# Kernel optimization log

Hardware: AMD Instinct MI355X
Metric: run time of the kernel (lower is better)

The kernel has to match this reference:

```python
import jax, jax.numpy as jnp
import numpy as np

N, E, D = 50000, 800000, 128
NODE_IN, EDGE_IN, STEPS = 19, 4, 5
EPS = 1e-5

def leaky(x):
    return jnp.where(x > 0, x, 0.05 * x)

def mlp3(x, W1, b1, W2, b2, W3, b3):
    x = leaky(x @ W1 + b1)
    x = leaky(x @ W2 + b2)
    return x @ W3 + b3

def layer_norm(x, g, b):
    m = jnp.mean(x, axis=-1, keepdims=True)
    v = jnp.var(x, axis=-1, keepdims=True)
    return (x - m) * jax.lax.rsqrt(v + EPS) * g + b

def batch_norm(x, g, b):
    # training-mode BatchNorm1d: biased batch stats over node dim
    m = jnp.mean(x, axis=0)
    v = jnp.var(x, axis=0)
    return (x - m) * jax.lax.rsqrt(v + EPS) * g + b

def gcn_conv(x, src, dst, W, b):
    # PyG GCNConv: add self loops, sym-normalize by deg^{-1/2}, aggregate at dst
    h = x @ W  # [N, D]
    deg = jax.ops.segment_sum(jnp.ones(E, x.dtype), dst, num_segments=N) + 1.0
    dis = jax.lax.rsqrt(deg)
    msg = h[src] * (dis[src] * dis[dst])[:, None]  # [E, D]
    agg = jax.ops.segment_sum(msg, dst, num_segments=N) + h * (dis * dis)[:, None]
    return agg + b


def setup_inputs() -> dict:
    key = jax.random.key(0)
    ks = iter(jax.random.split(key, 64))
    w = lambda shape: jax.random.normal(next(ks), shape, jnp.float32) * 0.05
    z = lambda: jnp.zeros((D,), jnp.float32)
    o = lambda: jnp.ones((D,), jnp.float32)
    inp = {
        'node_feat': jax.random.normal(next(ks), (N, NODE_IN), jnp.float32),
        'edge_feat': jax.random.normal(next(ks), (E, EDGE_IN), jnp.float32),
        'edge_index': jax.random.randint(next(ks), (2, E), 0, N, jnp.int32),
        'enc_node_W1': w((NODE_IN, D)), 'enc_node_b1': z(),
        'enc_node_W2': w((D, D)), 'enc_node_b2': z(),
        'enc_node_W3': w((D, D)), 'enc_node_b3': z(),
        'enc_node_ln_g': o(), 'enc_node_ln_b': z(),
        'enc_edge_W1': w((EDGE_IN, D)), 'enc_edge_b1': z(),
        'enc_edge_W2': w((D, D)), 'enc_edge_b2': z(),
        'enc_edge_W3': w((D, D)), 'enc_edge_b3': z(),
        'enc_edge_ln_g': o(), 'enc_edge_ln_b': z(),
        'proc_W': w((STEPS, 2, D, D)),
        'proc_b': jnp.zeros((STEPS, 2, D), jnp.float32),
        'proc_bn_g': jnp.ones((STEPS, D), jnp.float32),
        'proc_bn_b': jnp.zeros((STEPS, D), jnp.float32),
        'dec_W1': w((D, D)), 'dec_b1': z(),
        'dec_W2': w((D, D)), 'dec_b2': z(),
        'dec_W3': w((D, D)), 'dec_b3': z(),
        'dec_ln_g': o(), 'dec_ln_b': z(),
    }
    return inp


def reference(node_feat, edge_feat, edge_index,
              enc_node_W1, enc_node_b1, enc_node_W2, enc_node_b2, enc_node_W3, enc_node_b3,
              enc_node_ln_g, enc_node_ln_b,
              enc_edge_W1, enc_edge_b1, enc_edge_W2, enc_edge_b2, enc_edge_W3, enc_edge_b3,
              enc_edge_ln_g, enc_edge_ln_b,
              proc_W, proc_b, proc_bn_g, proc_bn_b,
              dec_W1, dec_b1, dec_W2, dec_b2, dec_W3, dec_b3, dec_ln_g, dec_ln_b):
    src, dst = edge_index[0], edge_index[1]
    # encode
    hn = layer_norm(mlp3(node_feat, enc_node_W1, enc_node_b1, enc_node_W2, enc_node_b2,
                         enc_node_W3, enc_node_b3), enc_node_ln_g, enc_node_ln_b)
    he = layer_norm(mlp3(edge_feat, enc_edge_W1, enc_edge_b1, enc_edge_W2, enc_edge_b2,
                         enc_edge_W3, enc_edge_b3), enc_edge_ln_g, enc_edge_ln_b)
    # scatter-mean edge features onto source nodes
    cnt = jax.ops.segment_sum(jnp.ones(E, hn.dtype), src, num_segments=N)
    hn = hn + jax.ops.segment_sum(he, src, num_segments=N) / jnp.maximum(cnt, 1.0)[:, None]
    # 5 residual GCN processor steps (GCNConv -> LeakyReLU -> BN -> GCNConv)
    for s in range(STEPS):
        x = gcn_conv(hn, src, dst, proc_W[s, 0], proc_b[s, 0])
        x = batch_norm(leaky(x), proc_bn_g[s], proc_bn_b[s])
        x = gcn_conv(x, src, dst, proc_W[s, 1], proc_b[s, 1])
        hn = hn + x
    # decode
    return layer_norm(mlp3(hn, dec_W1, dec_b1, dec_W2, dec_b2, dec_W3, dec_b3),
                      dec_ln_g, dec_ln_b)
```

## Files before the change

### kernel.cpp

```cpp
#include <hip/hip_runtime.h>

#define NN 50000
#define NE 800000
#define DD 128
#define LN_EPS 1e-5f

typedef __attribute__((ext_vector_type(8))) short v8s;
typedef __attribute__((ext_vector_type(4))) float f32x4;

__device__ __forceinline__ float leakyf(float x){ return x > 0.f ? x : 0.05f*x; }
__device__ __forceinline__ short f2bf(float f){
  unsigned u = __float_as_uint(f);
  u = (u + 0x7fffu + ((u >> 16) & 1u)) >> 16;
  return (short)u;
}
__device__ __forceinline__ float bf2f(unsigned short h){
  return __uint_as_float(((unsigned)h) << 16);
}
__device__ __forceinline__ short2 f2bf2v(float v){
  unsigned u = __float_as_uint(v);
  short hi = (short)(u >> 16);
  float lo = v - __uint_as_float(u & 0xffff0000u);
  return make_short2(hi, f2bf(lo));
}

__global__ void pack_w_kernel(const float* __restrict__ W, short* __restrict__ Wh,
                              short* __restrict__ Wl, int K, int Kp)
{
  int idx = blockIdx.x*256 + threadIdx.x;
  if (idx >= Kp*128) return;
  int k = idx >> 7, n = idx & 127;
  float v = (k < K) ? W[k*128 + n] : 0.f;
  short2 t = f2bf2v(v);
  size_t o = ((size_t)(k >> 3)*128 + n)*8 + (k & 7);
  Wh[o] = t.x; Wl[o] = t.y;
}

#define NPACK 11
struct PackArgs { const float* src[NPACK]; short* dh[NPACK]; short* dl[NPACK]; };

__global__ void pack_many_kernel(PackArgs pa)
{
  int m = blockIdx.y;
  int idx = blockIdx.x*256 + threadIdx.x;
  int k = idx >> 7, n = idx & 127;
  float v = pa.src[m][k*128 + n];
  short2 t = f2bf2v(v);
  size_t o = ((size_t)(k >> 3)*128 + n)*8 + (k & 7);
  pa.dh[m][o] = t.x; pa.dl[m][o] = t.y;
}

#define MFMA3(ah, al, bh, bl, ac) \
  ac = __builtin_amdgcn_mfma_f32_16x16x32_bf16(al, bh, ac, 0,0,0); \
  ac = __builtin_amdgcn_mfma_f32_16x16x32_bf16(ah, bl, ac, 0,0,0); \
  ac = __builtin_amdgcn_mfma_f32_16x16x32_bf16(ah, bh, ac, 0,0,0);

#define MFMA2(ah, bh, bl, ac) \
  ac = __builtin_amdgcn_mfma_f32_16x16x32_bf16(ah, bl, ac, 0,0,0); \
  ac = __builtin_amdgcn_mfma_f32_16x16x32_bf16(ah, bh, ac, 0,0,0);

#define SPLIT8(f0, f1, h, l) { \
  short2 t0 = f2bf2v(f0.x), t1 = f2bf2v(f0.y), t2 = f2bf2v(f0.z), t3 = f2bf2v(f0.w); \
  short2 t4 = f2bf2v(f1.x), t5 = f2bf2v(f1.y), t6 = f2bf2v(f1.z), t7 = f2bf2v(f1.w); \
  h[0]=t0.x; l[0]=t0.y; h[1]=t1.x; l[1]=t1.y; h[2]=t2.x; l[2]=t2.y; h[3]=t3.x; l[3]=t3.y; \
  h[4]=t4.x; l[4]=t4.y; h[5]=t5.x; l[5]=t5.y; h[6]=t6.x; l[6]=t6.y; h[7]=t7.x; l[7]=t7.y; }

template<int IN_W, bool SCATTER>
__global__ __launch_bounds__(256)
void mlp_mfma_kernel(const float* __restrict__ x, int nrows,
                     const short* __restrict__ W1h, const short* __restrict__ W1l,
                     const float* __restrict__ b1,
                     const short* __restrict__ W2h, const short* __restrict__ W2l,
                     const float* __restrict__ b2,
                     const short* __restrict__ W3h, const short* __restrict__ W3l,
                     const float* __restrict__ b3,
                     const float* __restrict__ g, const float* __restrict__ bb,
                     float* __restrict__ out,
                     const int* __restrict__ sidx,
                     const int* __restrict__ eperm)
{
  constexpr int L1K = (IN_W + 31) / 32;
  __shared__ __align__(16) short Hh[128*136];
  __shared__ float lnS[128][2], lnQ[128][2];
  __shared__ int sidx_s[128];
  __shared__ __align__(16) float4 xstage[SCATTER ? 128 : 1];

  const int tid  = threadIdx.x;
  const int lane = tid & 63, wave = tid >> 6;
  const int wr = wave >> 1, wc = wave & 1;
  const int quad = lane >> 4, low = lane & 15;
  const int row0 = blockIdx.x * 128;

  if (SCATTER) {
    if (tid < 128) {
      int e = eperm[row0 + tid];
      xstage[tid] = ((const float4*)x)[e];
      sidx_s[tid] = sidx[row0 + tid];
    }
    __syncthreads();
  }

  f32x4 acc[4][4];

  #pragma unroll
  for (int tm=0;tm<4;tm++)
    #pragma unroll
    for (int tn=0;tn<4;tn++) acc[tm][tn] = (f32x4)0.f;

  for (int ks = 0; ks < L1K; ks++) {
    v8s ah[4], al[4], bh[4], bl[4];
    #pragma unroll
    for (int tm=0;tm<4;tm++) {
      int lr = wr*64 + tm*16 + low;
      v8s h = (v8s)0, l = (v8s)0;
      if (SCATTER && IN_W == 4) {
        if (quad == 0) {
          float4 f = xstage[lr];
          short2 t0 = f2bf2v(f.x), t1 = f2bf2v(f.y), t2 = f2bf2v(f.z), t3 = f2bf2v(f.w);
          h[0]=t0.x; l[0]=t0.y; h[1]=t1.x; l[1]=t1.y;
          h[2]=t2.x; l[2]=t2.y; h[3]=t3.x; l[3]=t3.y;
        }
      } else if (IN_W % 32 == 0) {
        int r = row0 + lr;
        if (r < nrows) {
          const float* p = x + (size_t)r*IN_W + ks*32 + quad*8;
          float4 f0 = *(const float4*)p;
          float4 f1 = *(const float4*)(p + 4);
          SPLIT8(f0, f1, h, l);
        }
      } else {
        int r = row0 + lr;
        #pragma unroll
        for (int j=0;j<8;j++) {
          int k = ks*32 + quad*8 + j;
          if (k < IN_W && r < nrows) {
            short2 t = f2bf2v(x[(size_t)r*IN_W + k]);
            h[j] = t.x; l[j] = t.y;
          }
        }
      }
      ah[tm] = h; al[tm] = l;
    }
    #pragma unroll
    for (int tn=0;tn<4;tn++) {
      size_t o = ((size_t)(ks*4+quad)*128 + wc*64 + tn*16 + low)*8;
      bh[tn] = *(const v8s*)(W1h + o);
      bl[tn] = *(const v8s*)(W1l + o);
    }
    #pragma unroll
    for (int tm=0;tm<4;tm++)
      #pragma unroll
      for (int tn=0;tn<4;tn++) { MFMA3(ah[tm], al[tm], bh[tn], bl[tn], acc[tm][tn]); }
  }
  #pragma unroll
  for (int tn=0;tn<4;tn++) {
    float bv = b1[wc*64 + tn*16 + low];
    #pragma unroll
    for (int tm=0;tm<4;tm++)
      #pragma unroll
      for (int i=0;i<4;i++) {
        int idx = (wr*64+tm*16+quad*4+i)*136 + wc*64+tn*16+low;
        Hh[idx] = f2bf(leakyf(acc[tm][tn][i] + bv));
      }
  }
  __syncthreads();

  #pragma unroll
  for (int tm=0;tm<4;tm++)
    #pragma unroll
    for (int tn=0;tn<4;tn++) acc[tm][tn] = (f32x4)0.f;
  #pragma unroll
  for (int ks=0;ks<4;ks++) {
    v8s ah[4], bh[4], bl[4];
    #pragma unroll
    for (int tm=0;tm<4;tm++)
      ah[tm] = *(const v8s*)&Hh[(wr*64+tm*16+low)*136 + ks*32 + quad*8];
    #pragma unroll
    for (int tn=0;tn<4;tn++) {
      size_t o = ((size_t)(ks*4+quad)*128 + wc*64 + tn*16 + low)*8;
      bh[tn] = *(const v8s*)(W2h + o);
      bl[tn] = *(const v8s*)(W2l + o);
    }
    #pragma unroll
    for (int tm=0;tm<4;tm++)
      #pragma unroll
      for (int tn=0;tn<4;tn++) { MFMA2(ah[tm], bh[tn], bl[tn], acc[tm][tn]); }
  }
  __syncthreads();
  #pragma unroll
  for (int tn=0;tn<4;tn++) {
    float bv = b2[wc*64 + tn*16 + low];
    #pragma unroll
    for (int tm=0;tm<4;tm++)
      #pragma unroll
      for (int i=0;i<4;i++) {
        int idx = (wr*64+tm*16+quad*4+i)*136 + wc*64+tn*16+low;
        Hh[idx] = f2bf(leakyf(acc[tm][tn][i] + bv));
      }
  }
  __syncthreads();

  #pragma unroll
  for (int tm=0;tm<4;tm++)
    #pragma unroll
    for (int tn=0;tn<4;tn++) acc[tm][tn] = (f32x4)0.f;
  #pragma unroll
  for (int ks=0;ks<4;ks++) {
    v8s ah[4], bh[4], bl[4];
    #pragma unroll
    for (int tm=0;tm<4;tm++)
      ah[tm] = *(const v8s*)&Hh[(wr*64+tm*16+low)*136 + ks*32 + quad*8];
    #pragma unroll
    for (int tn=0;tn<4;tn++) {
      size_t o = ((size_t)(ks*4+quad)*128 + wc*64 + tn*16 + low)*8;
      bh[tn] = *(const v8s*)(W3h + o);
      bl[tn] = *(const v8s*)(W3l + o);
    }
    #pragma unroll
    for (int tm=0;tm<4;tm++)
      #pragma unroll
      for (int tn=0;tn<4;tn++) { MFMA2(ah[tm], bh[tn], bl[tn], acc[tm][tn]); }
  }
  #pragma unroll
  for (int tn=0;tn<4;tn++) {
    float bv = b3[wc*64 + tn*16 + low];
    #pragma unroll
    for (int tm=0;tm<4;tm++)
      #pragma unroll
      for (int i=0;i<4;i++) acc[tm][tn][i] += bv;
  }

  #pragma unroll
  for (int tm=0;tm<4;tm++)
    #pragma unroll
    for (int i=0;i<4;i++) {
      float s = acc[tm][0][i] + acc[tm][1][i] + acc[tm][2][i] + acc[tm][3][i];
      float q = acc[tm][0][i]*acc[tm][0][i] + acc[tm][1][i]*acc[tm][1][i]
              + acc[tm][2][i]*acc[tm][2][i] + acc[tm][3][i]*acc[tm][3][i];
      s += __shfl_xor(s, 1); q += __shfl_xor(q, 1);
      s += __shfl_xor(s, 2); q += __shfl_xor(q, 2);
      s += __shfl_xor(s, 4); q += __shfl_xor(q, 4);
      s += __shfl_xor(s, 8); q += __shfl_xor(q, 8);
      if (low == tm*4 + i) {
        int r = wr*64 + tm*16 + quad*4 + i;
        lnS[r][wc] = s; lnQ[r][wc] = q;
      }
    }
  __syncthreads();

  float g4[4], bb4[4];
  #pragma unroll
  for (int tn=0;tn<4;tn++) { int c = wc*64+tn*16+low; g4[tn] = g[c]; bb4[tn] = bb[c]; }

  #pragma unroll
  for (int tm=0;tm<4;tm++)
    #pragma unroll
    for (int i=0;i<4;i++) {
      int r = wr*64 + tm*16 + quad*4 + i;
      float s = lnS[r][0] + lnS[r][1];
      float q = lnQ[r][0] + lnQ[r][1];
      float m = s * (1.f/128.f);
      float var = q * (1.f/128.f) - m*m;
      float rs = rsqrtf(var + LN_EPS);
      int gr = row0 + r;
      if (!SCATTER && gr >= nrows) continue;
      #pragma unroll
      for (int tn=0;tn<4;tn++) {
        float v = (acc[tm][tn][i] - m) * rs * g4[tn] + bb4[tn];
        int c = wc*64 + tn*16 + low;
        if (SCATTER) Hh[r*132 + c] = f2bf(v);
        else         out[(size_t)gr*DD + c] = v;
      }
    }

  if (SCATTER) {
    __syncthreads();
    int col  = tid & 127;
    int rbeg = (tid >> 7) * 64, rend = rbeg + 64;
    float accv = bf2f((unsigned short)Hh[rbeg*132 + col]);
    int cur = sidx_s[rbeg];
    for (int r = rbeg + 1; r < rend; r++) {
      int sv = sidx_s[r];
      float hv = bf2f((unsigned short)Hh[r*132 + col]);
      if (sv != cur) {
        atomicAdd(&out[(size_t)cur*DD + col], accv);
        accv = hv; cur = sv;
      } else accv += hv;
    }
    atomicAdd(&out[(size_t)cur*DD + col], accv);
  }
}

__global__ __launch_bounds__(256)
void gemm_mfma_kernel(const float* __restrict__ x,
                      const short* __restrict__ Wh, const short* __restrict__ Wl,
                      const float* __restrict__ initv, const float* __restrict__ rowscale,
                      unsigned short* __restrict__ outbf, int nrows)
{
  const int tid  = threadIdx.x;
  const int lane = tid & 63, wave = tid >> 6;
  const int wr = wave >> 1, wc = wave & 1;
  const int quad = lane >> 4, low = lane & 15;
  const int row0 = blockIdx.x * 64;

  f32x4 acc[2][4];
  #pragma unroll
  for (int tm=0;tm<2;tm++)
    #pragma unroll
    for (int tn=0;tn<4;tn++) acc[tm][tn] = (f32x4)0.f;

  #pragma unroll
  for (int ks=0;ks<4;ks++) {
    v8s ah[2], al[2], bh[4], bl[4];
    #pragma unroll
    for (int tm=0;tm<2;tm++) {
      int r = row0 + wr*32 + tm*16 + low;
      v8s h = (v8s)0, l = (v8s)0;
      if (r < nrows) {
        const float* p = x + (size_t)r*DD + ks*32 + quad*8;
        float4 f0 = *(const float4*)p;
        float4 f1 = *(const float4*)(p + 4);
        SPLIT8(f0, f1, h, l);
      }
      ah[tm] = h; al[tm] = l;
    }
    #pragma unroll
    for (int tn=0;tn<4;tn++) {
      size_t o = ((size_t)(ks*4+quad)*128 + wc*64 + tn*16 + low)*8;
      bh[tn] = *(const v8s*)(Wh + o);
      bl[tn] = *(const v8s*)(Wl + o);
    }
    #pragma unroll
    for (int tm=0;tm<2;tm++)
      #pragma unroll
      for (int tn=0;tn<4;tn++) { MFMA3(ah[tm], al[tm], bh[tn], bl[tn], acc[tm][tn]); }
  }

  #pragma unroll
  for (int tm=0;tm<2;tm++)
    #pragma unroll
    for (int i=0;i<4;i++) {
      int gr = row0 + wr*32 + tm*16 + quad*4 + i;
      if (gr >= nrows) continue;
      float sc = rowscale ? rowscale[gr] : 1.f;
      #pragma unroll
      for (int tn=0;tn<4;tn++) {
        int c = wc*64 + tn*16 + low;
        float iv = initv ? initv[c] : 0.f;
        outbf[(size_t)gr*DD + c] = (unsigned short)f2bf((acc[tm][tn][i] + iv) * sc);
      }
    }
}

__global__ __launch_bounds__(256)
void gemm_bf_mfma_kernel(const unsigned short* __restrict__ xb,
                         const short* __restrict__ Wh, const short* __restrict__ Wl,
                         const float* __restrict__ initv, const float* __restrict__ rowscale,
                         unsigned short* __restrict__ outbf, int nrows)
{
  const int tid  = threadIdx.x;
  const int lane = tid & 63, wave = tid >> 6;
  const int wr = wave >> 1, wc = wave & 1;
  const int quad = lane >> 4, low = lane & 15;
  const int row0 = blockIdx.x * 64;

  f32x4 acc[2][4];
  #pragma unroll
  for (int tm=0;tm<2;tm++)
    #pragma unroll
    for (int tn=0;tn<4;tn++) acc[tm][tn] = (f32x4)0.f;

  #pragma unroll
  for (int ks=0;ks<4;ks++) {
    v8s ah[2], bh[4], bl[4];
    #pragma unroll
    for (int tm=0;tm<2;tm++) {
      int r = row0 + wr*32 + tm*16 + low;
      ah[tm] = (r < nrows) ? *(const v8s*)(xb + (size_t)r*DD + ks*32 + quad*8) : (v8s)0;
    }
    #pragma unroll
    for (int tn=0;tn<4;tn++) {
      size_t o = ((size_t)(ks*4+quad)*128 + wc*64 + tn*16 + low)*8;
      bh[tn] = *(const v8s*)(Wh + o);
      bl[tn] = *(const v8s*)(Wl + o);
    }
    #pragma unroll
    for (int tm=0;tm<2;tm++)
      #pragma unroll
      for (int tn=0;tn<4;tn++) { MFMA2(ah[tm], bh[tn], bl[tn], acc[tm][tn]); }
  }

  #pragma unroll
  for (int tm=0;tm<2;tm++)
    #pragma unroll
    for (int i=0;i<4;i++) {
      int gr = row0 + wr*32 + tm*16 + quad*4 + i;
      if (gr >= nrows) continue;
      float sc = rowscale ? rowscale[gr] : 1.f;
      #pragma unroll
      for (int tn=0;tn<4;tn++) {
        int c = wc*64 + tn*16 + low;
        float iv = initv ? initv[c] : 0.f;
        outbf[(size_t)gr*DD + c] = (unsigned short)f2bf((acc[tm][tn][i] + iv) * sc);
      }
    }
}

__global__ __launch_bounds__(256)
void gcn_agg_kernel(const unsigned* __restrict__ hb, const int* __restrict__ rowptr,
                    const int* __restrict__ csr_src, const float* __restrict__ dis,
                    const float* __restrict__ bias, const float* __restrict__ resid,
                    float* __restrict__ outf, unsigned* __restrict__ outb, int mode)
{
  const int wv = threadIdx.x >> 6, lane = threadIdx.x & 63;
  const int i = blockIdx.x*4 + wv;
  if (i >= NN) return;
  unsigned hv = hb[(size_t)i*64 + lane];
  float ax = bf2f((unsigned short)(hv & 0xffff)), ay = bf2f((unsigned short)(hv >> 16));
  const int beg = rowptr[i], end = rowptr[i+1];
  int j = beg;
  for (; j + 16 <= end; j += 16) {
    unsigned v[16];
    #pragma unroll
    for (int k=0;k<16;k++) v[k] = hb[(size_t)csr_src[j+k]*64 + lane];
    #pragma unroll
    for (int k=0;k<16;k++) {
      ax += bf2f((unsigned short)(v[k] & 0xffff));
      ay += bf2f((unsigned short)(v[k] >> 16));
    }
  }
  for (; j + 4 <= end; j += 4) {
    unsigned v[4];
    #pragma unroll
    for (int k=0;k<4;k++) v[k] = hb[(size_t)csr_src[j+k]*64 + lane];
    #pragma unroll
    for (int k=0;k<4;k++) {
      ax += bf2f((unsigned short)(v[k] & 0xffff));
      ay += bf2f((unsigned short)(v[k] >> 16));
    }
  }
  for (; j < end; j++) {
    unsigned v = hb[(size_t)csr_src[j]*64 + lane];
    ax += bf2f((unsigned short)(v & 0xffff));
    ay += bf2f((unsigned short)(v >> 16));
  }
  float di = dis[i];
  ax = ax*di + bias[2*lane]; ay = ay*di + bias[2*lane+1];
  size_t o = (size_t)i*64 + lane;
  if (mode == 0) {
    unsigned pk = ((unsigned)(unsigned short)f2bf(leakyf(ay)) << 16)
                |  (unsigned)(unsigned short)f2bf(leakyf(ax));
    outb[o] = pk;
  } else {
    float2 rs = ((const float2*)resid)[o];
    float2 r; r.x = rs.x + ax; r.y = rs.y + ay;
    ((float2*)outf)[o] = r;
  }
}

__global__ void count_kernel(const int* __restrict__ src, const int* __restrict__ dst,
                             int* __restrict__ cnt_src, int* __restrict__ deg_dst)
{
  int e = blockIdx.x*blockDim.x + threadIdx.x;
  if (e < NE) {
    atomicAdd(&cnt_src[src[e]], 1);
    atomicAdd(&deg_dst[dst[e]], 1);
  }
}

__global__ void nodeparams_kernel(const int* __restrict__ deg_dst, const int* __restrict__ cnt_src,
                                  float* __restrict__ dis, float* __restrict__ invcnt)
{
  int i = blockIdx.x*blockDim.x + threadIdx.x;
  if (i < NN) {
    dis[i] = rsqrtf((float)deg_dst[i] + 1.0f);
    invcnt[i] = 1.0f / fmaxf((float)cnt_src[i], 1.0f);
  }
}

__global__ void scan2_kernel(const int* __restrict__ a0, int* __restrict__ r0, int* __restrict__ n0,
                             const int* __restrict__ a1, int* __restrict__ r1, int* __restrict__ n1)
{
  const int* a = blockIdx.x ? a1 : a0;
  int* r = blockIdx.x ? r1 : r0;
  int* n = blockIdx.x ? n1 : n0;
  const int T = 256;
  int tid = threadIdx.x;
  int chunk = (NN + T - 1) / T;
  int begin = tid*chunk, end = begin + chunk; if (end > NN) end = NN; if (begin > NN) begin = NN;
  int s = 0;
  for (int i = begin; i < end; i++) s += a[i];
  __shared__ int ps[T];
  ps[tid] = s; __syncthreads();
  for (int off = 1; off < T; off <<= 1) {
    int v = 0;
    if (tid >= off) v = ps[tid - off];
    __syncthreads();
    if (tid >= off) ps[tid] += v;
    __syncthreads();
  }
  int base = (tid == 0) ? 0 : ps[tid-1];
  for (int i = begin; i < end; i++) { r[i] = base; n[i] = base; base += a[i]; }
  if (tid == T-1) r[NN] = base;
}

__global__ void fill_kernel(const int* __restrict__ src, const int* __restrict__ dst,
                            int* __restrict__ nextp, int* __restrict__ csr_src)
{
  int e = blockIdx.x*blockDim.x + threadIdx.x;
  if (e < NE) {
    int pos = atomicAdd(&nextp[dst[e]], 1);
    csr_src[pos] = src[e];
  }
}

__global__ void fill_src_kernel(const int* __restrict__ src, int* __restrict__ nexts,
                                int* __restrict__ eperm, int* __restrict__ srcsorted)
{
  int e = blockIdx.x*blockDim.x + threadIdx.x;
  if (e < NE) {
    int s = src[e];
    int pos = atomicAdd(&nexts[s], 1);
    eperm[pos] = e;
    srcsorted[pos] = s;
  }
}

__global__ void addmean_kernel(float* __restrict__ hn, const float* __restrict__ nodesum,
                               const float* __restrict__ invcnt)
{
  int t = blockIdx.x*blockDim.x + threadIdx.x;
  if (t < NN*DD) hn[t] += nodesum[t] * invcnt[t >> 7];
}

__global__ __launch_bounds__(256)
void bn_stats_kernel(const unsigned short* __restrict__ yb, float* __restrict__ sums)
{
  int col = threadIdx.x & 127, grp = threadIdx.x >> 7;
  float s = 0.f, ss = 0.f;
  for (int i = blockIdx.x*2 + grp; i < NN; i += gridDim.x*2) {
    float v = bf2f(yb[(size_t)i*DD + col]);
    s += v; ss += v*v;
  }
  __shared__ float ls[256], lss[256];
  ls[threadIdx.x] = s; lss[threadIdx.x] = ss;
  __syncthreads();
  if (grp == 0) {
    atomicAdd(&sums[col],      ls[col]  + ls[col+128]);
    atomicAdd(&sums[DD + col], lss[col] + lss[col+128]);
  }
}

__global__ __launch_bounds__(256)
void bn_fold_kernel(const float* __restrict__ sums, const float* __restrict__ g,
                    const float* __restrict__ b, const float* __restrict__ W2,
                    short* __restrict__ Wfh, short* __restrict__ Wfl,
                    float* __restrict__ cvec)
{
  __shared__ float scale_s[DD], shift_s[DD];
  int tid = threadIdx.x;
  if (tid < DD) {
    float m = sums[tid] / (float)NN;
    float var = sums[DD + tid] / (float)NN - m*m;
    float is = rsqrtf(var + LN_EPS);
    float sc = is * g[tid];
    scale_s[tid] = sc;
    shift_s[tid] = b[tid] - m * sc;
  }
  __syncthreads();
  int col = tid & 127, kh = tid >> 7;
  float cpart = 0.f;
  #pragma unroll
  for (int kk = 0; kk < 4; kk++) {
    int k = blockIdx.x*8 + kh*4 + kk;
    float w = W2[k*DD + col];
    short2 t = f2bf2v(w * scale_s[k]);
    size_t o = ((size_t)(k >> 3)*128 + col)*8 + (k & 7);
    Wfh[o] = t.x; Wfl[o] = t.y;
    cpart += shift_s[k] * w;
  }
  atomicAdd(&cvec[col], cpart);
}

extern "C" void kernel_launch(void* const* d_in, const int* in_sizes, int n_in,
                              void* d_out, int out_size, void* d_ws, size_t ws_size,
                              hipStream_t stream)
{
  const float* node_feat = (const float*)d_in[0];
  const float* edge_feat = (const float*)d_in[1];
  const int*   edge_index = (const int*)d_in[2];
  const int* src = edge_index;
  const int* dst = edge_index + NE;

  const float* enW1 = (const float*)d_in[3];  const float* enb1 = (const float*)d_in[4];
  const float* enW2 = (const float*)d_in[5];  const float* enb2 = (const float*)d_in[6];
  const float* enW3 = (const float*)d_in[7];  const float* enb3 = (const float*)d_in[8];
  const float* enlg = (const float*)d_in[9];  const float* enlb = (const float*)d_in[10];

  const float* eeW1 = (const float*)d_in[11]; const float* eeb1 = (const float*)d_in[12];
  const float* eeW2 = (const float*)d_in[13]; const float* eeb2 = (const float*)d_in[14];
  const float* eeW3 = (const float*)d_in[15]; const float* eeb3 = (const float*)d_in[16];
  const float* eelg = (const float*)d_in[17]; const float* eelb = (const float*)d_in[18];

  const float* procW = (const float*)d_in[19];
  const float* procB = (const float*)d_in[20];
  const float* bnG   = (const float*)d_in[21];
  const float* bnB   = (const float*)d_in[22];

  const float* dW1 = (const float*)d_in[23]; const float* db1 = (const float*)d_in[24];
  const float* dW2 = (const float*)d_in[25]; const float* db2 = (const float*)d_in[26];
  const float* dW3 = (const float*)d_in[27]; const float* db3 = (const float*)d_in[28];
  const float* dlg = (const float*)d_in[29]; const float* dlb = (const float*)d_in[30];

  char* ws = (char*)d_ws;
  size_t off = 0;
  auto alloc = [&](size_t bytes) -> void* {
    void* p = ws + off;
    off = (off + bytes + 255) & ~(size_t)255;
    return p;
  };
  float* hn     = (float*)alloc((size_t)NN*DD*4);
  float* esum   = (float*)alloc((size_t)NN*DD*4);
  unsigned short* hbf = (unsigned short*)alloc((size_t)NN*DD*2);
  unsigned short* ybf = (unsigned short*)alloc((size_t)NN*DD*2);
  float* dis    = (float*)alloc(NN*4);
  float* invcnt = (float*)alloc(NN*4);
  float* bnsums = (float*)alloc(3*DD*4);
  float* cvec   = bnsums + 2*DD;
  int* deg    = (int*)alloc(NN*4);
  int* cnt    = (int*)alloc(NN*4);
  int* rowptr = (int*)alloc((NN+1)*4);
  int* nextp  = (int*)alloc(NN*4);
  int* srow   = (int*)alloc((NN+1)*4);
  int* nexts  = (int*)alloc(NN*4);
  int* csr    = (int*)alloc((size_t)NE*4);
  int* eperm  = (int*)alloc((size_t)NE*4);
  int* srcsorted = (int*)alloc((size_t)NE*4);
  auto allocW = [&](int kp) { return (short*)alloc((size_t)kp*128*2); };
  short *pN1h=allocW(32),  *pN1l=allocW(32);
  short *pN2h=allocW(128), *pN2l=allocW(128);
  short *pN3h=allocW(128), *pN3l=allocW(128);
  short *pE1h=allocW(32),  *pE1l=allocW(32);
  short *pE2h=allocW(128), *pE2l=allocW(128);
  short *pE3h=allocW(128), *pE3l=allocW(128);
  short *pD1h=allocW(128), *pD1l=allocW(128);
  short *pD2h=allocW(128), *pD2l=allocW(128);
  short *pD3h=allocW(128), *pD3l=allocW(128);
  short *pP0h[5], *pP0l[5];
  for (int s = 0; s < 5; s++) { pP0h[s]=allocW(128); pP0l[s]=allocW(128); }
  short *pWfh=allocW(128), *pWfl=allocW(128);

  (void)hipMemsetAsync(deg, 0, NN*4, stream);
  (void)hipMemsetAsync(cnt, 0, NN*4, stream);
  (void)hipMemsetAsync(esum, 0, (size_t)NN*DD*4, stream);

  PackArgs pa;
  const float* s128[NPACK] = { enW2, enW3, eeW2, eeW3, dW1, dW2, dW3,
                               procW + 0*(size_t)DD*DD*2, procW + 1*(size_t)DD*DD*2,
                               procW + 2*(size_t)DD*DD*2, procW + 3*(size_t)DD*DD*2 };
  short* d128h[NPACK] = { pN2h, pN3h, pE2h, pE3h, pD1h, pD2h, pD3h, pP0h[0], pP0h[1], pP0h[2], pP0h[3] };
  short* d128l[NPACK] = { pN2l, pN3l, pE2l, pE3l, pD1l, pD2l, pD3l, pP0l[0], pP0l[1], pP0l[2], pP0l[3] };
  for (int m = 0; m < NPACK; m++) { pa.src[m]=s128[m]; pa.dh[m]=d128h[m]; pa.dl[m]=d128l[m]; }
  pack_many_kernel<<<dim3(64, NPACK), 256, 0, stream>>>(pa);
  const int G32 = (32*128+255)/256, G128 = (128*128+255)/256;
  pack_w_kernel<<<G32, 256, 0, stream>>>(enW1, pN1h, pN1l, 19, 32);
  pack_w_kernel<<<G32, 256, 0, stream>>>(eeW1, pE1h, pE1l, 4, 32);
  pack_w_kernel<<<G128,256, 0, stream>>>(procW + 4*(size_t)DD*DD*2, pP0h[4], pP0l[4], 128, 128);

  count_kernel<<<(NE+255)/256, 256, 0, stream>>>(src, dst, cnt, deg);
  nodeparams_kernel<<<(NN+255)/256, 256, 0, stream>>>(deg, cnt, dis, invcnt);
  scan2_kernel<<<2, 256, 0, stream>>>(deg, rowptr, nextp, cnt, srow, nexts);
  fill_kernel<<<(NE+255)/256, 256, 0, stream>>>(src, dst, nextp, csr);
  fill_src_kernel<<<(NE+255)/256, 256, 0, stream>>>(src, nexts, eperm, srcsorted);

  const int GN  = (NN + 127) / 128;
  const int GE  = NE / 128;
  const int GG  = (NN + 63) / 64;
  const int GA  = (NN + 3) / 4;

  mlp_mfma_kernel<19, false><<<GN, 256, 0, stream>>>(node_feat, NN,
      pN1h, pN1l, enb1, pN2h, pN2l, enb2, pN3h, pN3l, enb3, enlg, enlb, hn,
      nullptr, nullptr);
  mlp_mfma_kernel<4, true><<<GE, 256, 0, stream>>>(edge_feat, NE,
      pE1h, pE1l, eeb1, pE2h, pE2l, eeb2, pE3h, pE3l, eeb3, eelg, eelb, esum,
      srcsorted, eperm);
  addmean_kernel<<<(NN*DD+255)/256, 256, 0, stream>>>(hn, esum, invcnt);

  for (int s = 0; s < 5; s++) {
    const float* Wc2 = procW + (size_t)(s*2+1)*DD*DD;
    const float* b0  = procB + (size_t)(s*2+0)*DD;
    const float* b1p = procB + (size_t)(s*2+1)*DD;

    gemm_mfma_kernel<<<GG, 256, 0, stream>>>(hn, pP0h[s], pP0l[s], nullptr, dis, hbf, NN);
    gcn_agg_kernel<<<GA, 256, 0, stream>>>((const unsigned*)hbf, rowptr, csr, dis,
                                           b0, nullptr, nullptr, (unsigned*)ybf, 0);
    (void)hipMemsetAsync(bnsums, 0, 3*DD*4, stream);
    bn_stats_kernel<<<512, 256, 0, stream>>>(ybf, bnsums);
    bn_fold_kernel<<<16, 256, 0, stream>>>(bnsums, bnG + s*DD, bnB + s*DD, Wc2, pWfh, pWfl, cvec);
    gemm_bf_mfma_kernel<<<GG, 256, 0, stream>>>(ybf, pWfh, pWfl, cvec, dis, hbf, NN);
    gcn_agg_kernel<<<GA, 256, 0, stream>>>((const unsigned*)hbf, rowptr, csr, dis,
                                           b1p, hn, hn, nullptr, 1);
  }

  mlp_mfma_kernel<128, false><<<GN, 256, 0, stream>>>(hn, NN,
      pD1h, pD1l, db1, pD2h, pD2l, db2, pD3h, pD3l, db3, dlg, dlb, (float*)d_out,
      nullptr, nullptr);
}
```

Measured before the change: 1.413 ms.

## Use packed bf16 conversions, pre-split edge features, and vectorize addmean

Replaces the software bf16 rounding with the hardware v_cvt_pk_bf16_f32 instruction and a byte-permute for the high/low split across the MLP, GEMM and aggregation epilogues. Edge features are split into bf16 hi/lo once at staging time instead of per-use. The scatter-sum loop now handles column pairs, and the addmean kernel is vectorized to float4. Bias loads are hoisted out of the row loops and the wave index is made uniform. These trim ALU work in the conversion-heavy epilogues, at the cost of relying on inline asm and on the hardware rounding matching the old software rounding.

Measured after the change: 1.333 ms. 1.06x faster.

```diff
diff --git a/kernel.cpp b/kernel.cpp
--- a/kernel.cpp
+++ b/kernel.cpp
@@ -6,7 +6,10 @@
 #define LN_EPS 1e-5f
 
 typedef __attribute__((ext_vector_type(8))) short v8s;
+typedef __attribute__((ext_vector_type(4))) unsigned v4u;
 typedef __attribute__((ext_vector_type(4))) float f32x4;
+
+union CvtHL { v4u u; v8s s; };
 
 __device__ __forceinline__ float leakyf(float x){ return x > 0.f ? x : 0.05f*x; }
 __device__ __forceinline__ short f2bf(float f){
@@ -16,6 +19,14 @@
 }
 __device__ __forceinline__ float bf2f(unsigned short h){
   return __uint_as_float(((unsigned)h) << 16);
+}
+__device__ __forceinline__ unsigned cvt_pk_bf16(float a, float b){
+  unsigned r;
+  asm("v_cvt_pk_bf16_f32 %0, %1, %2" : "=v"(r) : "v"(a), "v"(b));
+  return r;
+}
+__device__ __forceinline__ unsigned pack_hi16(unsigned u0, unsigned u1){
+  return __builtin_amdgcn_perm(u1, u0, 0x07060302u);
 }
 __device__ __forceinline__ short2 f2bf2v(float v){
   unsigned u = __float_as_uint(v);
@@ -60,10 +71,16 @@
   ac = __builtin_amdgcn_mfma_f32_16x16x32_bf16(ah, bh, ac, 0,0,0);
 
 #define SPLIT8(f0, f1, h, l) { \
-  short2 t0 = f2bf2v(f0.x), t1 = f2bf2v(f0.y), t2 = f2bf2v(f0.z), t3 = f2bf2v(f0.w); \
-  short2 t4 = f2bf2v(f1.x), t5 = f2bf2v(f1.y), t6 = f2bf2v(f1.z), t7 = f2bf2v(f1.w); \
-  h[0]=t0.x; l[0]=t0.y; h[1]=t1.x; l[1]=t1.y; h[2]=t2.x; l[2]=t2.y; h[3]=t3.x; l[3]=t3.y; \
-  h[4]=t4.x; l[4]=t4.y; h[5]=t5.x; l[5]=t5.y; h[6]=t6.x; l[6]=t6.y; h[7]=t7.x; l[7]=t7.y; }
+  unsigned u0=__float_as_uint(f0.x), u1=__float_as_uint(f0.y), u2=__float_as_uint(f0.z), u3=__float_as_uint(f0.w); \
+  unsigned u4=__float_as_uint(f1.x), u5=__float_as_uint(f1.y), u6=__float_as_uint(f1.z), u7=__float_as_uint(f1.w); \
+  CvtHL ch_, cl_; \
+  ch_.u = (v4u){ pack_hi16(u0,u1), pack_hi16(u2,u3), pack_hi16(u4,u5), pack_hi16(u6,u7) }; \
+  cl_.u = (v4u){ \
+    cvt_pk_bf16(f0.x-__uint_as_float(u0&0xffff0000u), f0.y-__uint_as_float(u1&0xffff0000u)), \
+    cvt_pk_bf16(f0.z-__uint_as_float(u2&0xffff0000u), f0.w-__uint_as_float(u3&0xffff0000u)), \
+    cvt_pk_bf16(f1.x-__uint_as_float(u4&0xffff0000u), f1.y-__uint_as_float(u5&0xffff0000u)), \
+    cvt_pk_bf16(f1.z-__uint_as_float(u6&0xffff0000u), f1.w-__uint_as_float(u7&0xffff0000u)) }; \
+  h = ch_.s; l = cl_.s; }
 
 template<int IN_W, bool SCATTER>
 __global__ __launch_bounds__(256)
@@ -83,7 +100,7 @@
   __shared__ __align__(16) short Hh[128*136];
   __shared__ float lnS[128][2], lnQ[128][2];
   __shared__ int sidx_s[128];
-  __shared__ __align__(16) float4 xstage[SCATTER ? 128 : 1];
+  __shared__ __align__(16) uint4 xstage[SCATTER ? 128 : 1];
 
   const int tid  = threadIdx.x;
   const int lane = tid & 63, wave = tid >> 6;
@@ -94,7 +111,15 @@
   if (SCATTER) {
     if (tid < 128) {
       int e = eperm[row0 + tid];
-      xstage[tid] = ((const float4*)x)[e];
+      float4 f = ((const float4*)x)[e];
+      unsigned u0=__float_as_uint(f.x), u1=__float_as_uint(f.y);
+      unsigned u2=__float_as_uint(f.z), u3=__float_as_uint(f.w);
+      uint4 st;
+      st.x = pack_hi16(u0,u1);
+      st.y = pack_hi16(u2,u3);
+      st.z = cvt_pk_bf16(f.x-__uint_as_float(u0&0xffff0000u), f.y-__uint_as_float(u1&0xffff0000u));
+      st.w = cvt_pk_bf16(f.z-__uint_as_float(u2&0xffff0000u), f.w-__uint_as_float(u3&0xffff0000u));
+      xstage[tid] = st;
       sidx_s[tid] = sidx[row0 + tid];
     }
     __syncthreads();
@@ -115,10 +140,11 @@
       v8s h = (v8s)0, l = (v8s)0;
       if (SCATTER && IN_W == 4) {
         if (quad == 0) {
-          float4 f = xstage[lr];
-          short2 t0 = f2bf2v(f.x), t1 = f2bf2v(f.y), t2 = f2bf2v(f.z), t3 = f2bf2v(f.w);
-          h[0]=t0.x; l[0]=t0.y; h[1]=t1.x; l[1]=t1.y;
-          h[2]=t2.x; l[2]=t2.y; h[3]=t3.x; l[3]=t3.y;
+          uint4 st = xstage[lr];
+          CvtHL ch_, cl_;
+          ch_.u = (v4u){ st.x, st.y, 0u, 0u };
+          cl_.u = (v4u){ st.z, st.w, 0u, 0u };
+          h = ch_.s; l = cl_.s;
         }
       } else if (IN_W % 32 == 0) {
         int r = row0 + lr;
@@ -156,12 +182,15 @@
   for (int tn=0;tn<4;tn++) {
     float bv = b1[wc*64 + tn*16 + low];
     #pragma unroll
-    for (int tm=0;tm<4;tm++)
-      #pragma unroll
-      for (int i=0;i<4;i++) {
-        int idx = (wr*64+tm*16+quad*4+i)*136 + wc*64+tn*16+low;
-        Hh[idx] = f2bf(leakyf(acc[tm][tn][i] + bv));
-      }
+    for (int tm=0;tm<4;tm++) {
+      unsigned p01 = cvt_pk_bf16(leakyf(acc[tm][tn][0]+bv), leakyf(acc[tm][tn][1]+bv));
+      unsigned p23 = cvt_pk_bf16(leakyf(acc[tm][tn][2]+bv), leakyf(acc[tm][tn][3]+bv));
+      int base = (wr*64+tm*16+quad*4)*136 + wc*64+tn*16+low;
+      Hh[base]     = (short)p01;
+      Hh[base+136] = (short)(p01>>16);
+      Hh[base+272] = (short)p23;
+      Hh[base+408] = (short)(p23>>16);
+    }
   }
   __syncthreads();
 
@@ -191,12 +220,15 @@
   for (int tn=0;tn<4;tn++) {
     float bv = b2[wc*64 + tn*16 + low];
     #pragma unroll
-    for (int tm=0;tm<4;tm++)
-      #pragma unroll
-      for (int i=0;i<4;i++) {
-        int idx = (wr*64+tm*16+quad*4+i)*136 + wc*64+tn*16+low;
-        Hh[idx] = f2bf(leakyf(acc[tm][tn][i] + bv));
-      }
+    for (int tm=0;tm<4;tm++) {
+      unsigned p01 = cvt_pk_bf16(leakyf(acc[tm][tn][0]+bv), leakyf(acc[tm][tn][1]+bv));
+      unsigned p23 = cvt_pk_bf16(leakyf(acc[tm][tn][2]+bv), leakyf(acc[tm][tn][3]+bv));
+      int base = (wr*64+tm*16+quad*4)*136 + wc*64+tn*16+low;
+      Hh[base]     = (short)p01;
+      Hh[base+136] = (short)(p01>>16);
+      Hh[base+272] = (short)p23;
+      Hh[base+408] = (short)(p23>>16);
+    }
   }
   __syncthreads();
 
@@ -264,30 +296,49 @@
       float rs = rsqrtf(var + LN_EPS);
       int gr = row0 + r;
       if (!SCATTER && gr >= nrows) continue;
-      #pragma unroll
-      for (int tn=0;tn<4;tn++) {
-        float v = (acc[tm][tn][i] - m) * rs * g4[tn] + bb4[tn];
-        int c = wc*64 + tn*16 + low;
-        if (SCATTER) Hh[r*132 + c] = f2bf(v);
-        else         out[(size_t)gr*DD + c] = v;
+      float v0 = (acc[tm][0][i] - m) * rs * g4[0] + bb4[0];
+      float v1 = (acc[tm][1][i] - m) * rs * g4[1] + bb4[1];
+      float v2 = (acc[tm][2][i] - m) * rs * g4[2] + bb4[2];
+      float v3 = (acc[tm][3][i] - m) * rs * g4[3] + bb4[3];
+      if (SCATTER) {
+        unsigned p01 = cvt_pk_bf16(v0, v1), p23 = cvt_pk_bf16(v2, v3);
+        int base = r*132 + wc*64 + low;
+        Hh[base]    = (short)p01;
+        Hh[base+16] = (short)(p01>>16);
+        Hh[base+32] = (short)p23;
+        Hh[base+48] = (short)(p23>>16);
+      } else {
+        size_t ob = (size_t)gr*DD + wc*64 + low;
+        out[ob]    = v0;
+        out[ob+16] = v1;
+        out[ob+32] = v2;
+        out[ob+48] = v3;
       }
     }
 
   if (SCATTER) {
     __syncthreads();
-    int col  = tid & 127;
-    int rbeg = (tid >> 7) * 64, rend = rbeg + 64;
-    float accv = bf2f((unsigned short)Hh[rbeg*132 + col]);
+    const unsigned* H32 = (const unsigned*)Hh;
+    int cp = tid & 63;
+    int gI = tid >> 6;
+    int rbeg = gI*32, rend = rbeg + 32;
+    unsigned pv = H32[rbeg*66 + cp];
+    float a0 = __uint_as_float(pv << 16), a1 = __uint_as_float(pv & 0xffff0000u);
     int cur = sidx_s[rbeg];
     for (int r = rbeg + 1; r < rend; r++) {
       int sv = sidx_s[r];
-      float hv = bf2f((unsigned short)Hh[r*132 + col]);
+      unsigned hv = H32[r*66 + cp];
       if (sv != cur) {
-        atomicAdd(&out[(size_t)cur*DD + col], accv);
-        accv = hv; cur = sv;
-      } else accv += hv;
-    }
-    atomicAdd(&out[(size_t)cur*DD + col], accv);
+        atomicAdd(&out[(size_t)cur*DD + 2*cp],     a0);
+        atomicAdd(&out[(size_t)cur*DD + 2*cp + 1], a1);
+        a0 = __uint_as_float(hv << 16); a1 = __uint_as_float(hv & 0xffff0000u);
+        cur = sv;
+      } else {
+        a0 += __uint_as_float(hv << 16); a1 += __uint_as_float(hv & 0xffff0000u);
+      }
+    }
+    atomicAdd(&out[(size_t)cur*DD + 2*cp],     a0);
+    atomicAdd(&out[(size_t)cur*DD + 2*cp + 1], a1);
   }
 }
 
@@ -336,6 +387,10 @@
       for (int tn=0;tn<4;tn++) { MFMA3(ah[tm], al[tm], bh[tn], bl[tn], acc[tm][tn]); }
   }
 
+  float iv4[4];
+  #pragma unroll
+  for (int tn=0;tn<4;tn++) iv4[tn] = initv ? initv[wc*64 + tn*16 + low] : 0.f;
+
   #pragma unroll
   for (int tm=0;tm<2;tm++)
     #pragma unroll
@@ -343,12 +398,16 @@
       int gr = row0 + wr*32 + tm*16 + quad*4 + i;
       if (gr >= nrows) continue;
       float sc = rowscale ? rowscale[gr] : 1.f;
-      #pragma unroll
-      for (int tn=0;tn<4;tn++) {
-        int c = wc*64 + tn*16 + low;
-        float iv = initv ? initv[c] : 0.f;
-        outbf[(size_t)gr*DD + c] = (unsigned short)f2bf((acc[tm][tn][i] + iv) * sc);
-      }
+      float v0 = (acc[tm][0][i] + iv4[0]) * sc;
+      float v1 = (acc[tm][1][i] + iv4[1]) * sc;
+      float v2 = (acc[tm][2][i] + iv4[2]) * sc;
+      float v3 = (acc[tm][3][i] + iv4[3]) * sc;
+      unsigned p01 = cvt_pk_bf16(v0, v1), p23 = cvt_pk_bf16(v2, v3);
+      size_t base = (size_t)gr*DD + wc*64 + low;
+      outbf[base]    = (unsigned short)p01;
+      outbf[base+16] = (unsigned short)(p01>>16);
+      outbf[base+32] = (unsigned short)p23;
+      outbf[base+48] = (unsigned short)(p23>>16);
     }
 }
 
@@ -390,6 +449,10 @@
       for (int tn=0;tn<4;tn++) { MFMA2(ah[tm], bh[tn], bl[tn], acc[tm][tn]); }
   }
 
+  float iv4[4];
+  #pragma unroll
+  for (int tn=0;tn<4;tn++) iv4[tn] = initv ? initv[wc*64 + tn*16 + low] : 0.f;
+
   #pragma unroll
   for (int tm=0;tm<2;tm++)
     #pragma unroll
@@ -397,12 +460,16 @@
       int gr = row0 + wr*32 + tm*16 + quad*4 + i;
       if (gr >= nrows) continue;
       float sc = rowscale ? rowscale[gr] : 1.f;
-      #pragma unroll
-      for (int tn=0;tn<4;tn++) {
-        int c = wc*64 + tn*16 + low;
-        float iv = initv ? initv[c] : 0.f;
-        outbf[(size_t)gr*DD + c] = (unsigned short)f2bf((acc[tm][tn][i] + iv) * sc);
-      }
+      float v0 = (acc[tm][0][i] + iv4[0]) * sc;
+      float v1 = (acc[tm][1][i] + iv4[1]) * sc;
+      float v2 = (acc[tm][2][i] + iv4[2]) * sc;
+      float v3 = (acc[tm][3][i] + iv4[3]) * sc;
+      unsigned p01 = cvt_pk_bf16(v0, v1), p23 = cvt_pk_bf16(v2, v3);
+      size_t base = (size_t)gr*DD + wc*64 + low;
+      outbf[base]    = (unsigned short)p01;
+      outbf[base+16] = (unsigned short)(p01>>16);
+      outbf[base+32] = (unsigned short)p23;
+      outbf[base+48] = (unsigned short)(p23>>16);
     }
 }
 
@@ -412,7 +479,8 @@
                     const float* __restrict__ bias, const float* __restrict__ resid,
                     float* __restrict__ outf, unsigned* __restrict__ outb, int mode)
 {
-  const int wv = threadIdx.x >> 6, lane = threadIdx.x & 63;
+  const int wv = __builtin_amdgcn_readfirstlane(threadIdx.x >> 6);
+  const int lane = threadIdx.x & 63;
   const int i = blockIdx.x*4 + wv;
   if (i >= NN) return;
   unsigned hv = hb[(size_t)i*64 + lane];
@@ -448,9 +516,7 @@
   ax = ax*di + bias[2*lane]; ay = ay*di + bias[2*lane+1];
   size_t o = (size_t)i*64 + lane;
   if (mode == 0) {
-    unsigned pk = ((unsigned)(unsigned short)f2bf(leakyf(ay)) << 16)
-                |  (unsigned)(unsigned short)f2bf(leakyf(ax));
-    outb[o] = pk;
+    outb[o] = cvt_pk_bf16(leakyf(ax), leakyf(ay));
   } else {
     float2 rs = ((const float2*)resid)[o];
     float2 r; r.x = rs.x + ax; r.y = rs.y + ay;
@@ -530,7 +596,13 @@
                                const float* __restrict__ invcnt)
 {
   int t = blockIdx.x*blockDim.x + threadIdx.x;
-  if (t < NN*DD) hn[t] += nodesum[t] * invcnt[t >> 7];
+  if (t < NN*DD/4) {
+    float4 a = ((const float4*)hn)[t];
+    float4 b = ((const float4*)nodesum)[t];
+    float ic = invcnt[t >> 5];
+    a.x += b.x*ic; a.y += b.y*ic; a.z += b.z*ic; a.w += b.w*ic;
+    ((float4*)hn)[t] = a;
+  }
 }
 
 __global__ __launch_bounds__(256)
@@ -684,7 +756,7 @@
   mlp_mfma_kernel<4, true><<<GE, 256, 0, stream>>>(edge_feat, NE,
       pE1h, pE1l, eeb1, pE2h, pE2l, eeb2, pE3h, pE3l, eeb3, eelg, eelb, esum,
       srcsorted, eperm);
-  addmean_kernel<<<(NN*DD+255)/256, 256, 0, stream>>>(hn, esum, invcnt);
+  addmean_kernel<<<(NN*DD/4+255)/256, 256, 0, stream>>>(hn, esum, invcnt);
 
   for (int s = 0; s < 5; s++) {
     const float* Wc2 = procW + (size_t)(s*2+1)*DD*DD;
```
